# Kernel tuning notes

Hardware: AMD Instinct MI355X
Metric: run time of the kernel (lower is better)

Reference implementation:

```python
import jax, jax.numpy as jnp
import numpy as np

N = 256            # state_space_size
BF = (4, 4, 4)     # branching_factors
T = 128            # time steps
D_IN = 64          # input_size
D_T = 64           # time_embedding_size
BATCH = 16
NUM_NODES = N * 4 * 4 * 4  # 16384


def setup_inputs() -> dict:
    key = jax.random.key(0)
    ks = jax.random.split(key, 20)

    def lin_w(k, out_d, in_d):
        return jax.random.normal(k, (out_d, in_d), jnp.float32) / np.sqrt(in_d)

    inp = {
        "x": jax.random.normal(ks[0], (BATCH, T, N), jnp.float32),
        "t_embeddings_schedule": jax.random.normal(ks[1], (T, D_T), jnp.float32),
        "input_vector": jax.random.normal(ks[2], (BATCH, T, D_IN), jnp.float32),
        # Fanout node params
        "Wa": lin_w(ks[3], NUM_NODES, N),
        "ba": jnp.zeros((NUM_NODES,), jnp.float32),
        "Wt": lin_w(ks[4], NUM_NODES, D_T),
        "Wi": lin_w(ks[5], NUM_NODES, D_IN),
        # Node with bf[:3]=[4,4,4]: reduces last 4 -> [N,4,4]
        "w3": jax.random.normal(ks[6], (N, 4, 4, 4), jnp.float32) * np.sqrt(2.0 / (4 + N * 16)),
        "tW3": lin_w(ks[7], N * 16, D_T),
        "tb3": jnp.zeros((N * 16,), jnp.float32),
        # Node with bf[:2]=[4,4]
        "w2": jax.random.normal(ks[8], (N, 4, 4), jnp.float32) * np.sqrt(2.0 / (4 + N * 4)),
        "tW2": lin_w(ks[9], N * 4, D_T),
        "tb2": jnp.zeros((N * 4,), jnp.float32),
        # Node with bf[:1]=[4]
        "w1": jax.random.normal(ks[10], (N, 4), jnp.float32) * np.sqrt(2.0 / (4 + N)),
        "tW1": lin_w(ks[11], N, D_T),
        "tb1": jnp.zeros((N,), jnp.float32),
    }
    return inp


def _node(act, t_emb, w, tW, tb):
    # act: [..., T, N, *bf]; w: [N, *bf]; reduce last branching dim
    tproj = (t_emb @ tW.T + tb).reshape(t_emb.shape[0], *w.shape[:-1])  # [T, N, *bf[:-1]]
    pre = (w * act).sum(-1) + tproj  # broadcast over leading batch dims
    return jax.nn.softplus(pre)


def reference(x, t_embeddings_schedule, input_vector, Wa, ba, Wt, Wi,
              w3, tW3, tb3, w2, tW2, tb2, w1, tW1, tb1):
    t_emb = t_embeddings_schedule
    # Fanout: [B, T, N] -> [B, T, N, 4, 4, 4]
    pre = x @ Wa.T + ba + (t_emb @ Wt.T) + input_vector @ Wi.T  # [B, T, NUM_NODES]
    act = jax.nn.softplus(pre.reshape(*pre.shape[:-1], N, *BF))
    # Tree: deepest node first (insert-at-1 order in original)
    act = _node(act, t_emb, w3, tW3, tb3)  # [B, T, N, 4, 4]
    act = _node(act, t_emb, w2, tW2, tb2)  # [B, T, N, 4]
    act = _node(act, t_emb, w1, tW1, tb1)  # [B, T, N]
    return act
```

## Files before the change

kernel.cpp:

```cpp
#include <hip/hip_runtime.h>

typedef __attribute__((ext_vector_type(16))) float f32x16;
typedef __attribute__((ext_vector_type(8))) __bf16 bf16x8;
typedef __attribute__((ext_vector_type(8))) unsigned short u16x8;

__device__ __forceinline__ unsigned short f2bf(float f) {
    unsigned int u = __float_as_uint(f);
    u += 0x7fffu + ((u >> 16) & 1u);
    return (unsigned short)(u >> 16);
}

__device__ __forceinline__ float softplus_f(float x) {
    float e = __expf(-fabsf(x));
    return fmaf(__log2f(1.0f + e), 0.69314718056f, fmaxf(x, 0.0f));
}

typedef __attribute__((address_space(3))) void lds_void_t;
typedef __attribute__((address_space(1))) void glb_void_t;

__device__ __forceinline__ void load16_to_lds(const void* g, const void* l) {
    __builtin_amdgcn_global_load_lds((glb_void_t*)(unsigned long long)g,
                                     (lds_void_t*)(unsigned int)(unsigned long long)l,
                                     16, 0, 0);
}

#define REPACK_NB 2
#define REPACK_BLOCKS 1728
__global__ __launch_bounds__(256) void repack(
        const float* __restrict__ x, const float* __restrict__ iv,
        const float* __restrict__ temb,
        const float* __restrict__ Wa, const float* __restrict__ Wi,
        const float* __restrict__ Wt,
        unsigned short* __restrict__ Abf ) {
    const int stride = REPACK_BLOCKS * 256;
    const int tid0 = blockIdx.x * 256 + threadIdx.x;
    float4 f[REPACK_NB][2];
    #pragma unroll
    for (int c = 0; c < REPACK_NB; ++c) {
        const int idx = tid0 + c * stride;
        const bool isA = idx < 98304;
        const int widx = isA ? idx : idx - 98304;
        const int row = widx / 48;
        const int kk  = (widx % 48) * 8;
        const float* p0 = isA ? (x    + (size_t)row * 256) : (Wa + (size_t)row * 256);
        const float* p1 = isA ? (iv   + (size_t)row * 64)  : (Wi + (size_t)row * 64);
        const float* p2 = isA ? (temb + (size_t)(row & 127) * 64) : (Wt + (size_t)row * 64);
        const float* src = (kk < 256) ? (p0 + kk) : ((kk < 320) ? (p1 + kk - 256) : (p2 + kk - 320));
        f[c][0] = ((const float4*)src)[0];
        f[c][1] = ((const float4*)src)[1];
    }
    #pragma unroll
    for (int c = 0; c < REPACK_NB; ++c) {
        const int idx = tid0 + c * stride;
        const bool isA = idx < 98304;
        const int widx = isA ? idx : idx - 98304;
        const int row = widx / 48;
        const int ch  = widx % 48;
        const size_t dst = isA ? (size_t)(((row >> 5) * 48 + ch) * 32 + (row & 31))
                               : (size_t)idx;
        u16x8 o;
        o[0] = f2bf(f[c][0].x); o[1] = f2bf(f[c][0].y); o[2] = f2bf(f[c][0].z); o[3] = f2bf(f[c][0].w);
        o[4] = f2bf(f[c][1].x); o[5] = f2bf(f[c][1].y); o[6] = f2bf(f[c][1].z); o[7] = f2bf(f[c][1].w);
        *(u16x8*)(Abf + dst * 8) = o;
    }
}

__global__ __launch_bounds__(256) void tproj(
        const float* __restrict__ temb,
        const float* __restrict__ tW3, const float* __restrict__ tb3,
        const float* __restrict__ tW2, const float* __restrict__ tb2,
        const float* __restrict__ tW1, const float* __restrict__ tb1,
        float* __restrict__ tp3T, float* __restrict__ tp2T, float* __restrict__ tp1T) {
    __shared__ float se[32 * 64];
    const int tid = threadIdx.x;
    const int tbase = blockIdx.y * 32;
    for (int i = tid; i < 32 * 64; i += 256) se[i] = temb[tbase * 64 + i];
    __syncthreads();
    const int j = blockIdx.x * 64 + (tid >> 2);
    const float* W; const float* bias; float* outp; int jl;
    if      (j < 4096) { W = tW3; bias = tb3; outp = tp3T; jl = j; }
    else if (j < 5120) { W = tW2; bias = tb2; outp = tp2T; jl = j - 4096; }
    else               { W = tW1; bias = tb1; outp = tp1T; jl = j - 5120; }
    float4 wreg[16];
    const float4* wrow = (const float4*)(W + (size_t)jl * 64);
    #pragma unroll
    for (int k = 0; k < 16; ++k) wreg[k] = wrow[k];
    const float b = bias[jl];
    #pragma unroll
    for (int s = 0; s < 8; ++s) {
        const int tl = (tid & 3) + s * 4;
        const float4* e4 = (const float4*)&se[tl * 64];
        float a = b;
        #pragma unroll
        for (int k = 0; k < 16; ++k) {
            float4 e = e4[k];
            a += wreg[k].x * e.x + wreg[k].y * e.y + wreg[k].z * e.z + wreg[k].w * e.w;
        }
        outp[(size_t)jl * 128 + tbase + tl] = a;
    }
}

__global__ __launch_bounds__(256, 3)
void fused_gemm_tree(const unsigned short* __restrict__ Wbf,
                     const unsigned short* __restrict__ Abf,
                     const float* __restrict__ ba,
                     const float* __restrict__ tp3T, const float* __restrict__ tp2T,
                     const float* __restrict__ tp1T,
                     const float* __restrict__ w3, const float* __restrict__ w2,
                     const float* __restrict__ w1,
                     float* __restrict__ out) {
    __shared__ unsigned short sW[128 * 64];

    const int tid  = threadIdx.x;
    const int wave = tid >> 6;
    const int lane = tid & 63;
    const int wr = wave >> 1;
    const int wc = wave & 1;
    const int lane31 = lane & 31;
    const int h = lane >> 5;

    const int node0 = blockIdx.x * 128;
    const int m0    = blockIdx.y * 128;

    f32x16 acc[2][2];
    #pragma unroll
    for (int fm = 0; fm < 2; ++fm)
        #pragma unroll
        for (int s2 = 0; s2 < 4; ++s2) {
            const float4 b4 = *(const float4*)&ba[node0 + wr * 64 + fm * 32 + 8 * s2 + 4 * h];
            #pragma unroll
            for (int l = 0; l < 4; ++l) {
                acc[fm][0][s2 * 4 + l] = ((const float*)&b4)[l];
                acc[fm][1][s2 * 4 + l] = ((const float*)&b4)[l];
            }
        }

    const unsigned short* aBase = Wbf + (size_t)node0 * 384;
    const int wrow0 = wr * 64 + lane31;

    const int mtBase = blockIdx.y * 4 + wc * 2;
    const unsigned short* bC0 = Abf + (((size_t)(mtBase + 0) * 48 + h) * 32 + lane31) * 8;
    const unsigned short* bC1 = Abf + (((size_t)(mtBase + 1) * 48 + h) * 32 + lane31) * 8;

    for (int k0 = 0; k0 < 384; k0 += 64) {
        __syncthreads();
        #pragma unroll
        for (int rr = 0; rr < 4; ++rr) {
            const int p = rr * 256 + tid;
            const int row = p >> 3;
            const int kchunk = (p & 7) ^ (row & 7);
            load16_to_lds(aBase + (size_t)row * 384 + k0 + kchunk * 8,
                          &sW[(size_t)(rr * 256 + wave * 64) * 8]);
        }
        bf16x8 bfr[2][4];
        const int cbase = k0 >> 3;
        #pragma unroll
        for (int s = 0; s < 4; ++s) {
            bfr[0][s] = *(const bf16x8*)(bC0 + (size_t)(cbase + 2 * s) * 256);
            bfr[1][s] = *(const bf16x8*)(bC1 + (size_t)(cbase + 2 * s) * 256);
        }
        __syncthreads();

        #pragma unroll
        for (int s = 0; s < 4; ++s) {
            const int kc = s * 2 + h;
            const int slot = (kc ^ (lane31 & 7)) * 8;
            bf16x8 af[2];
            #pragma unroll
            for (int fm = 0; fm < 2; ++fm)
                af[fm] = *(const bf16x8*)&sW[(wrow0 + fm * 32) * 64 + slot];
            #pragma unroll
            for (int fm = 0; fm < 2; ++fm)
                #pragma unroll
                for (int cf = 0; cf < 2; ++cf)
                    acc[fm][cf] = __builtin_amdgcn_mfma_f32_32x32x16_bf16(af[fm], bfr[cf][s], acc[fm][cf], 0, 0, 0);
        }
    }

    const int n = blockIdx.x * 2 + wr;
    const int t0 = wc * 64 + lane31;

    float4 w3v[2][4];
    #pragma unroll
    for (int fm = 0; fm < 2; ++fm)
        #pragma unroll
        for (int s2 = 0; s2 < 4; ++s2)
            w3v[fm][s2] = *(const float4*)&w3[n * 64 + fm * 32 + 8 * s2 + 4 * h];

    float w2v[4][2], w1v[4];
    #pragma unroll
    for (int i = 0; i < 4; ++i) {
        #pragma unroll
        for (int s2b = 0; s2b < 2; ++s2b)
            w2v[i][s2b] = w2[n * 16 + i * 4 + 2 * s2b + h];
        w1v[i] = w1[n * 4 + i];
    }
    float tp3v[2][2][4];
    #pragma unroll
    for (int fm = 0; fm < 2; ++fm)
        #pragma unroll
        for (int cf = 0; cf < 2; ++cf) {
            const int t = t0 + cf * 32;
            #pragma unroll
            for (int s2 = 0; s2 < 4; ++s2) {
                const int i  = fm * 2 + (s2 >> 1);
                const int jj = 2 * (s2 & 1) + h;
                tp3v[fm][cf][s2] = tp3T[(size_t)((n * 4 + i) * 4 + jj) * 128 + t];
            }
        }
    const int th = t0 + h * 32;
    float tp2h[2][2];
    #pragma unroll
    for (int fm = 0; fm < 2; ++fm)
        #pragma unroll
        for (int b = 0; b < 2; ++b)
            tp2h[fm][b] = tp2T[(size_t)(n * 4 + fm * 2 + b) * 128 + th];
    const float tp1h = tp1T[(size_t)n * 128 + th];

    float s1h = 0.0f;
    #pragma unroll
    for (int fm = 0; fm < 2; ++fm) {
        #pragma unroll
        for (int b = 0; b < 2; ++b) {
            float cs[2];
            #pragma unroll
            for (int cf = 0; cf < 2; ++cf) {
                float c = 0.0f;
                #pragma unroll
                for (int s2b = 0; s2b < 2; ++s2b) {
                    const int s2 = 2 * b + s2b;
                    float p3 = 0.0f;
                    const float* wv = (const float*)&w3v[fm][s2];
                    #pragma unroll
                    for (int l = 0; l < 4; ++l) {
                        float a0 = softplus_f(acc[fm][cf][s2 * 4 + l]);
                        p3 = fmaf(a0, wv[l], p3);
                    }
                    float a3 = softplus_f(p3 + tp3v[fm][cf][s2]);
                    c = fmaf(a3, w2v[fm * 2 + b][s2b], c);
                }
                cs[cf] = c;
            }
            const float Q0 = cs[0] + __shfl_xor(cs[0], 32);
            const float Q1 = cs[1] + __shfl_xor(cs[1], 32);
            const float Qh = h ? Q1 : Q0;
            const float a2 = softplus_f(Qh + tp2h[fm][b]);
            s1h = fmaf(a2, w1v[fm * 2 + b], s1h);
        }
    }
    out[(size_t)(m0 + th) * 256 + n] = softplus_f(s1h + tp1h);
}

extern "C" void kernel_launch(void* const* d_in, const int* in_sizes, int n_in,
                              void* d_out, int out_size, void* d_ws, size_t ws_size,
                              hipStream_t stream) {
    const float* x    = (const float*)d_in[0];
    const float* temb = (const float*)d_in[1];
    const float* iv   = (const float*)d_in[2];
    const float* Wa   = (const float*)d_in[3];
    const float* ba   = (const float*)d_in[4];
    const float* Wt   = (const float*)d_in[5];
    const float* Wi   = (const float*)d_in[6];
    const float* w3   = (const float*)d_in[7];
    const float* tW3  = (const float*)d_in[8];
    const float* tb3  = (const float*)d_in[9];
    const float* w2   = (const float*)d_in[10];
    const float* tW2  = (const float*)d_in[11];
    const float* tb2  = (const float*)d_in[12];
    const float* w1   = (const float*)d_in[13];
    const float* tW1  = (const float*)d_in[14];
    const float* tb1  = (const float*)d_in[15];
    float* out = (float*)d_out;

    char* ws = (char*)d_ws;
    unsigned short* Abf = (unsigned short*)(ws);
    unsigned short* Wbf = (unsigned short*)(ws + 1572864);
    float* tp3T = (float*)(ws + 14155776);
    float* tp2T = (float*)(ws + 16252928);
    float* tp1T = (float*)(ws + 16777216);

    repack<<<dim3(REPACK_BLOCKS), dim3(256), 0, stream>>>(x, iv, temb, Wa, Wi, Wt, Abf);
    tproj<<<dim3(84, 4), dim3(256), 0, stream>>>(temb, tW3, tb3, tW2, tb2, tW1, tb1,
                                                 tp3T, tp2T, tp1T);
    fused_gemm_tree<<<dim3(128, 16), dim3(256), 0, stream>>>(Wbf, Abf, ba, tp3T, tp2T, tp1T,
                                                             w3, w2, w1, out);
}
```

Measured before the change: 149.3 us.

## Tile-pack weights in repack and feed MFMA from global, merge prep kernels

Merges the repack and tproj kernels into one prep launch. Prep now writes the weight matrix in the same 32-row tiled layout as the activations. With that layout the GEMM loads both operands straight from global memory into registers and drops the LDS staging and its barriers. The aim is to cut launch overhead and synchronisation, at the cost of losing LDS reuse of weight tiles across the waves in a block, which puts more load on L2.

After: 173.5 us. 16.2% more time.

```diff
diff --git a/kernel.cpp b/kernel.cpp
--- a/kernel.cpp
+++ b/kernel.cpp
@@ -15,25 +15,56 @@
     return fmaf(__log2f(1.0f + e), 0.69314718056f, fmaxf(x, 0.0f));
 }
 
-typedef __attribute__((address_space(3))) void lds_void_t;
-typedef __attribute__((address_space(1))) void glb_void_t;
-
-__device__ __forceinline__ void load16_to_lds(const void* g, const void* l) {
-    __builtin_amdgcn_global_load_lds((glb_void_t*)(unsigned long long)g,
-                                     (lds_void_t*)(unsigned int)(unsigned long long)l,
-                                     16, 0, 0);
-}
-
 #define REPACK_NB 2
 #define REPACK_BLOCKS 1728
-__global__ __launch_bounds__(256) void repack(
+#define TPROJ_BLOCKS 336
+#define PREP_BLOCKS (REPACK_BLOCKS + TPROJ_BLOCKS)
+__global__ __launch_bounds__(256) void prep(
         const float* __restrict__ x, const float* __restrict__ iv,
         const float* __restrict__ temb,
         const float* __restrict__ Wa, const float* __restrict__ Wi,
         const float* __restrict__ Wt,
-        unsigned short* __restrict__ Abf ) {
+        const float* __restrict__ tW3, const float* __restrict__ tb3,
+        const float* __restrict__ tW2, const float* __restrict__ tb2,
+        const float* __restrict__ tW1, const float* __restrict__ tb1,
+        unsigned short* __restrict__ Abf ,
+        float* __restrict__ tp3T, float* __restrict__ tp2T, float* __restrict__ tp1T) {
+    __shared__ float se[32 * 64];
+    const int tid = threadIdx.x;
+
+    if (blockIdx.x < TPROJ_BLOCKS) {
+        const int bx = blockIdx.x % 84;
+        const int by = blockIdx.x / 84;
+        const int tbase = by * 32;
+        for (int i = tid; i < 32 * 64; i += 256) se[i] = temb[tbase * 64 + i];
+        __syncthreads();
+        const int j = bx * 64 + (tid >> 2);
+        const float* W; const float* bias; float* outp; int jl;
+        if      (j < 4096) { W = tW3; bias = tb3; outp = tp3T; jl = j; }
+        else if (j < 5120) { W = tW2; bias = tb2; outp = tp2T; jl = j - 4096; }
+        else               { W = tW1; bias = tb1; outp = tp1T; jl = j - 5120; }
+        float4 wreg[16];
+        const float4* wrow = (const float4*)(W + (size_t)jl * 64);
+        #pragma unroll
+        for (int k = 0; k < 16; ++k) wreg[k] = wrow[k];
+        const float b = bias[jl];
+        #pragma unroll
+        for (int s = 0; s < 8; ++s) {
+            const int tl = (tid & 3) + s * 4;
+            const float4* e4 = (const float4*)&se[tl * 64];
+            float a = b;
+            #pragma unroll
+            for (int k = 0; k < 16; ++k) {
+                float4 e = e4[k];
+                a += wreg[k].x * e.x + wreg[k].y * e.y + wreg[k].z * e.z + wreg[k].w * e.w;
+            }
+            outp[(size_t)jl * 128 + tbase + tl] = a;
+        }
+        return;
+    }
+
     const int stride = REPACK_BLOCKS * 256;
-    const int tid0 = blockIdx.x * 256 + threadIdx.x;
+    const int tid0 = (blockIdx.x - TPROJ_BLOCKS) * 256 + tid;
     float4 f[REPACK_NB][2];
     #pragma unroll
     for (int c = 0; c < REPACK_NB; ++c) {
@@ -56,8 +87,8 @@
         const int widx = isA ? idx : idx - 98304;
         const int row = widx / 48;
         const int ch  = widx % 48;
-        const size_t dst = isA ? (size_t)(((row >> 5) * 48 + ch) * 32 + (row & 31))
-                               : (size_t)idx;
+        const size_t dst = (size_t)(isA ? 0 : 98304) +
+                           (size_t)(((row >> 5) * 48 + ch) * 32 + (row & 31));
         u16x8 o;
         o[0] = f2bf(f[c][0].x); o[1] = f2bf(f[c][0].y); o[2] = f2bf(f[c][0].z); o[3] = f2bf(f[c][0].w);
         o[4] = f2bf(f[c][1].x); o[5] = f2bf(f[c][1].y); o[6] = f2bf(f[c][1].z); o[7] = f2bf(f[c][1].w);
@@ -65,52 +96,15 @@
     }
 }
 
-__global__ __launch_bounds__(256) void tproj(
-        const float* __restrict__ temb,
-        const float* __restrict__ tW3, const float* __restrict__ tb3,
-        const float* __restrict__ tW2, const float* __restrict__ tb2,
-        const float* __restrict__ tW1, const float* __restrict__ tb1,
-        float* __restrict__ tp3T, float* __restrict__ tp2T, float* __restrict__ tp1T) {
-    __shared__ float se[32 * 64];
-    const int tid = threadIdx.x;
-    const int tbase = blockIdx.y * 32;
-    for (int i = tid; i < 32 * 64; i += 256) se[i] = temb[tbase * 64 + i];
-    __syncthreads();
-    const int j = blockIdx.x * 64 + (tid >> 2);
-    const float* W; const float* bias; float* outp; int jl;
-    if      (j < 4096) { W = tW3; bias = tb3; outp = tp3T; jl = j; }
-    else if (j < 5120) { W = tW2; bias = tb2; outp = tp2T; jl = j - 4096; }
-    else               { W = tW1; bias = tb1; outp = tp1T; jl = j - 5120; }
-    float4 wreg[16];
-    const float4* wrow = (const float4*)(W + (size_t)jl * 64);
-    #pragma unroll
-    for (int k = 0; k < 16; ++k) wreg[k] = wrow[k];
-    const float b = bias[jl];
-    #pragma unroll
-    for (int s = 0; s < 8; ++s) {
-        const int tl = (tid & 3) + s * 4;
-        const float4* e4 = (const float4*)&se[tl * 64];
-        float a = b;
-        #pragma unroll
-        for (int k = 0; k < 16; ++k) {
-            float4 e = e4[k];
-            a += wreg[k].x * e.x + wreg[k].y * e.y + wreg[k].z * e.z + wreg[k].w * e.w;
-        }
-        outp[(size_t)jl * 128 + tbase + tl] = a;
-    }
-}
-
 __global__ __launch_bounds__(256, 3)
-void fused_gemm_tree(const unsigned short* __restrict__ Wbf,
-                     const unsigned short* __restrict__ Abf,
+void fused_gemm_tree(const unsigned short* __restrict__ Wf,
+                     const unsigned short* __restrict__ Af,
                      const float* __restrict__ ba,
                      const float* __restrict__ tp3T, const float* __restrict__ tp2T,
                      const float* __restrict__ tp1T,
                      const float* __restrict__ w3, const float* __restrict__ w2,
                      const float* __restrict__ w1,
                      float* __restrict__ out) {
-    __shared__ unsigned short sW[128 * 64];
-
     const int tid  = threadIdx.x;
     const int wave = tid >> 6;
     const int lane = tid & 63;
@@ -135,46 +129,24 @@
             }
         }
 
-    const unsigned short* aBase = Wbf + (size_t)node0 * 384;
-    const int wrow0 = wr * 64 + lane31;
-
+    const int ntBase = blockIdx.x * 4 + wr * 2;
     const int mtBase = blockIdx.y * 4 + wc * 2;
-    const unsigned short* bC0 = Abf + (((size_t)(mtBase + 0) * 48 + h) * 32 + lane31) * 8;
-    const unsigned short* bC1 = Abf + (((size_t)(mtBase + 1) * 48 + h) * 32 + lane31) * 8;
-
-    for (int k0 = 0; k0 < 384; k0 += 64) {
-        __syncthreads();
-        #pragma unroll
-        for (int rr = 0; rr < 4; ++rr) {
-            const int p = rr * 256 + tid;
-            const int row = p >> 3;
-            const int kchunk = (p & 7) ^ (row & 7);
-            load16_to_lds(aBase + (size_t)row * 384 + k0 + kchunk * 8,
-                          &sW[(size_t)(rr * 256 + wave * 64) * 8]);
-        }
-        bf16x8 bfr[2][4];
-        const int cbase = k0 >> 3;
-        #pragma unroll
-        for (int s = 0; s < 4; ++s) {
-            bfr[0][s] = *(const bf16x8*)(bC0 + (size_t)(cbase + 2 * s) * 256);
-            bfr[1][s] = *(const bf16x8*)(bC1 + (size_t)(cbase + 2 * s) * 256);
-        }
-        __syncthreads();
-
-        #pragma unroll
-        for (int s = 0; s < 4; ++s) {
-            const int kc = s * 2 + h;
-            const int slot = (kc ^ (lane31 & 7)) * 8;
-            bf16x8 af[2];
-            #pragma unroll
-            for (int fm = 0; fm < 2; ++fm)
-                af[fm] = *(const bf16x8*)&sW[(wrow0 + fm * 32) * 64 + slot];
-            #pragma unroll
-            for (int fm = 0; fm < 2; ++fm)
-                #pragma unroll
-                for (int cf = 0; cf < 2; ++cf)
-                    acc[fm][cf] = __builtin_amdgcn_mfma_f32_32x32x16_bf16(af[fm], bfr[cf][s], acc[fm][cf], 0, 0, 0);
-        }
+    const unsigned short* aC0 = Wf + (((size_t)(ntBase + 0) * 48 + h) * 32 + lane31) * 8;
+    const unsigned short* aC1 = Wf + (((size_t)(ntBase + 1) * 48 + h) * 32 + lane31) * 8;
+    const unsigned short* bC0 = Af + (((size_t)(mtBase + 0) * 48 + h) * 32 + lane31) * 8;
+    const unsigned short* bC1 = Af + (((size_t)(mtBase + 1) * 48 + h) * 32 + lane31) * 8;
+
+    #pragma unroll
+    for (int c = 0; c < 48; c += 2) {
+        const size_t off = (size_t)c * 256;
+        bf16x8 a0 = *(const bf16x8*)(aC0 + off);
+        bf16x8 a1 = *(const bf16x8*)(aC1 + off);
+        bf16x8 b0 = *(const bf16x8*)(bC0 + off);
+        bf16x8 b1 = *(const bf16x8*)(bC1 + off);
+        acc[0][0] = __builtin_amdgcn_mfma_f32_32x32x16_bf16(a0, b0, acc[0][0], 0, 0, 0);
+        acc[0][1] = __builtin_amdgcn_mfma_f32_32x32x16_bf16(a0, b1, acc[0][1], 0, 0, 0);
+        acc[1][0] = __builtin_amdgcn_mfma_f32_32x32x16_bf16(a1, b0, acc[1][0], 0, 0, 0);
+        acc[1][1] = __builtin_amdgcn_mfma_f32_32x32x16_bf16(a1, b1, acc[1][1], 0, 0, 0);
     }
 
     const int n = blockIdx.x * 2 + wr;
@@ -279,9 +251,9 @@
     float* tp2T = (float*)(ws + 16252928);
     float* tp1T = (float*)(ws + 16777216);
 
-    repack<<<dim3(REPACK_BLOCKS), dim3(256), 0, stream>>>(x, iv, temb, Wa, Wi, Wt, Abf);
-    tproj<<<dim3(84, 4), dim3(256), 0, stream>>>(temb, tW3, tb3, tW2, tb2, tW1, tb1,
-                                                 tp3T, tp2T, tp1T);
+    prep<<<dim3(PREP_BLOCKS), dim3(256), 0, stream>>>(x, iv, temb, Wa, Wi, Wt,
+                                                      tW3, tb3, tW2, tb2, tW1, tb1,
+                                                      Abf, tp3T, tp2T, tp1T);
     fused_gemm_tree<<<dim3(128, 16), dim3(256), 0, stream>>>(Wbf, Abf, ba, tp3T, tp2T, tp1T,
                                                              w3, w2, w1, out);
 }
```

## Double-buffer LDS in GEMM loop and fuse repack with tproj kernel

Applied to the files above, without the earlier changes.

The GEMM main loop now uses two LDS buffers, issuing the async global-to-LDS load for the next K tile before computing on the current one, and drops one barrier per iteration. The repack and time-projection kernels are merged into a single launch with block-index dispatch, saving a launch and letting both run concurrently. LDS usage per block doubles, which could affect occupancy.

After: 143.8 us. -3.7%, faster.

```diff
diff --git a/kernel.cpp b/kernel.cpp
--- a/kernel.cpp
+++ b/kernel.cpp
@@ -26,14 +26,54 @@
 
 #define REPACK_NB 2
 #define REPACK_BLOCKS 1728
-__global__ __launch_bounds__(256) void repack(
+#define TPROJ_BLOCKS 336
+#define PREP_BLOCKS (REPACK_BLOCKS + TPROJ_BLOCKS)
+__global__ __launch_bounds__(256) void prep(
         const float* __restrict__ x, const float* __restrict__ iv,
         const float* __restrict__ temb,
         const float* __restrict__ Wa, const float* __restrict__ Wi,
         const float* __restrict__ Wt,
-        unsigned short* __restrict__ Abf ) {
+        const float* __restrict__ tW3, const float* __restrict__ tb3,
+        const float* __restrict__ tW2, const float* __restrict__ tb2,
+        const float* __restrict__ tW1, const float* __restrict__ tb1,
+        unsigned short* __restrict__ Abf ,
+        float* __restrict__ tp3T, float* __restrict__ tp2T, float* __restrict__ tp1T) {
+    __shared__ float se[32 * 64];
+    const int tid = threadIdx.x;
+
+    if (blockIdx.x < TPROJ_BLOCKS) {
+        const int bx = blockIdx.x % 84;
+        const int by = blockIdx.x / 84;
+        const int tbase = by * 32;
+        for (int i = tid; i < 32 * 64; i += 256) se[i] = temb[tbase * 64 + i];
+        __syncthreads();
+        const int j = bx * 64 + (tid >> 2);
+        const float* W; const float* bias; float* outp; int jl;
+        if      (j < 4096) { W = tW3; bias = tb3; outp = tp3T; jl = j; }
+        else if (j < 5120) { W = tW2; bias = tb2; outp = tp2T; jl = j - 4096; }
+        else               { W = tW1; bias = tb1; outp = tp1T; jl = j - 5120; }
+        float4 wreg[16];
+        const float4* wrow = (const float4*)(W + (size_t)jl * 64);
+        #pragma unroll
+        for (int k = 0; k < 16; ++k) wreg[k] = wrow[k];
+        const float b = bias[jl];
+        #pragma unroll
+        for (int s = 0; s < 8; ++s) {
+            const int tl = (tid & 3) + s * 4;
+            const float4* e4 = (const float4*)&se[tl * 64];
+            float a = b;
+            #pragma unroll
+            for (int k = 0; k < 16; ++k) {
+                float4 e = e4[k];
+                a += wreg[k].x * e.x + wreg[k].y * e.y + wreg[k].z * e.z + wreg[k].w * e.w;
+            }
+            outp[(size_t)jl * 128 + tbase + tl] = a;
+        }
+        return;
+    }
+
     const int stride = REPACK_BLOCKS * 256;
-    const int tid0 = blockIdx.x * 256 + threadIdx.x;
+    const int tid0 = (blockIdx.x - TPROJ_BLOCKS) * 256 + tid;
     float4 f[REPACK_NB][2];
     #pragma unroll
     for (int c = 0; c < REPACK_NB; ++c) {
@@ -65,41 +105,6 @@
     }
 }
 
-__global__ __launch_bounds__(256) void tproj(
-        const float* __restrict__ temb,
-        const float* __restrict__ tW3, const float* __restrict__ tb3,
-        const float* __restrict__ tW2, const float* __restrict__ tb2,
-        const float* __restrict__ tW1, const float* __restrict__ tb1,
-        float* __restrict__ tp3T, float* __restrict__ tp2T, float* __restrict__ tp1T) {
-    __shared__ float se[32 * 64];
-    const int tid = threadIdx.x;
-    const int tbase = blockIdx.y * 32;
-    for (int i = tid; i < 32 * 64; i += 256) se[i] = temb[tbase * 64 + i];
-    __syncthreads();
-    const int j = blockIdx.x * 64 + (tid >> 2);
-    const float* W; const float* bias; float* outp; int jl;
-    if      (j < 4096) { W = tW3; bias = tb3; outp = tp3T; jl = j; }
-    else if (j < 5120) { W = tW2; bias = tb2; outp = tp2T; jl = j - 4096; }
-    else               { W = tW1; bias = tb1; outp = tp1T; jl = j - 5120; }
-    float4 wreg[16];
-    const float4* wrow = (const float4*)(W + (size_t)jl * 64);
-    #pragma unroll
-    for (int k = 0; k < 16; ++k) wreg[k] = wrow[k];
-    const float b = bias[jl];
-    #pragma unroll
-    for (int s = 0; s < 8; ++s) {
-        const int tl = (tid & 3) + s * 4;
-        const float4* e4 = (const float4*)&se[tl * 64];
-        float a = b;
-        #pragma unroll
-        for (int k = 0; k < 16; ++k) {
-            float4 e = e4[k];
-            a += wreg[k].x * e.x + wreg[k].y * e.y + wreg[k].z * e.z + wreg[k].w * e.w;
-        }
-        outp[(size_t)jl * 128 + tbase + tl] = a;
-    }
-}
-
 __global__ __launch_bounds__(256, 3)
 void fused_gemm_tree(const unsigned short* __restrict__ Wbf,
                      const unsigned short* __restrict__ Abf,
@@ -109,7 +114,7 @@
                      const float* __restrict__ w3, const float* __restrict__ w2,
                      const float* __restrict__ w1,
                      float* __restrict__ out) {
-    __shared__ unsigned short sW[128 * 64];
+    __shared__ unsigned short sW[2][128 * 64];
 
     const int tid  = threadIdx.x;
     const int wave = tid >> 6;
@@ -142,16 +147,25 @@
     const unsigned short* bC0 = Abf + (((size_t)(mtBase + 0) * 48 + h) * 32 + lane31) * 8;
     const unsigned short* bC1 = Abf + (((size_t)(mtBase + 1) * 48 + h) * 32 + lane31) * 8;
 
-    for (int k0 = 0; k0 < 384; k0 += 64) {
-        __syncthreads();
-        #pragma unroll
-        for (int rr = 0; rr < 4; ++rr) {
-            const int p = rr * 256 + tid;
-            const int row = p >> 3;
-            const int kchunk = (p & 7) ^ (row & 7);
-            load16_to_lds(aBase + (size_t)row * 384 + k0 + kchunk * 8,
-                          &sW[(size_t)(rr * 256 + wave * 64) * 8]);
-        }
+    int srow[4], skch[4];
+    #pragma unroll
+    for (int rr = 0; rr < 4; ++rr) {
+        const int p = rr * 256 + tid;
+        srow[rr] = p >> 3;
+        skch[rr] = (p & 7) ^ (srow[rr] & 7);
+    }
+    #define STAGE_A(K0, BB)                                                        \
+        _Pragma("unroll")                                                          \
+        for (int rr = 0; rr < 4; ++rr)                                             \
+            load16_to_lds(aBase + (size_t)srow[rr] * 384 + (K0) + skch[rr] * 8,    \
+                          &sW[BB][(size_t)(rr * 256 + wave * 64) * 8]);
+
+    STAGE_A(0, 0);
+    __syncthreads();
+
+    #pragma unroll
+    for (int it = 0; it < 6; ++it) {
+        const int k0 = it * 64;
         bf16x8 bfr[2][4];
         const int cbase = k0 >> 3;
         #pragma unroll
@@ -159,22 +173,21 @@
             bfr[0][s] = *(const bf16x8*)(bC0 + (size_t)(cbase + 2 * s) * 256);
             bfr[1][s] = *(const bf16x8*)(bC1 + (size_t)(cbase + 2 * s) * 256);
         }
-        __syncthreads();
-
+        if (it < 5) { STAGE_A(k0 + 64, (it + 1) & 1); }
         #pragma unroll
         for (int s = 0; s < 4; ++s) {
             const int kc = s * 2 + h;
-            const int slot = (kc ^ (lane31 & 7)) * 8;
+            const int slot = (kc ^ (lane & 7)) * 8;
             bf16x8 af[2];
             #pragma unroll
             for (int fm = 0; fm < 2; ++fm)
-                af[fm] = *(const bf16x8*)&sW[(wrow0 + fm * 32) * 64 + slot];
-            #pragma unroll
-            for (int fm = 0; fm < 2; ++fm)
-                #pragma unroll
-                for (int cf = 0; cf < 2; ++cf)
-                    acc[fm][cf] = __builtin_amdgcn_mfma_f32_32x32x16_bf16(af[fm], bfr[cf][s], acc[fm][cf], 0, 0, 0);
-        }
+                af[fm] = *(const bf16x8*)&sW[it & 1][(wrow0 + fm * 32) * 64 + slot];
+            acc[0][0] = __builtin_amdgcn_mfma_f32_32x32x16_bf16(af[0], bfr[0][s], acc[0][0], 0, 0, 0);
+            acc[0][1] = __builtin_amdgcn_mfma_f32_32x32x16_bf16(af[0], bfr[1][s], acc[0][1], 0, 0, 0);
+            acc[1][0] = __builtin_amdgcn_mfma_f32_32x32x16_bf16(af[1], bfr[0][s], acc[1][0], 0, 0, 0);
+            acc[1][1] = __builtin_amdgcn_mfma_f32_32x32x16_bf16(af[1], bfr[1][s], acc[1][1], 0, 0, 0);
+        }
+        if (it < 5) __syncthreads();
     }
 
     const int n = blockIdx.x * 2 + wr;
@@ -279,9 +292,9 @@
     float* tp2T = (float*)(ws + 16252928);
     float* tp1T = (float*)(ws + 16777216);
 
-    repack<<<dim3(REPACK_BLOCKS), dim3(256), 0, stream>>>(x, iv, temb, Wa, Wi, Wt, Abf);
-    tproj<<<dim3(84, 4), dim3(256), 0, stream>>>(temb, tW3, tb3, tW2, tb2, tW1, tb1,
-                                                 tp3T, tp2T, tp1T);
+    prep<<<dim3(PREP_BLOCKS), dim3(256), 0, stream>>>(x, iv, temb, Wa, Wi, Wt,
+                                                      tW3, tb3, tW2, tb2, tW1, tb1,
+                                                      Abf, tp3T, tp2T, tp1T);
     fused_gemm_tree<<<dim3(128, 16), dim3(256), 0, stream>>>(Wbf, Abf, ba, tp3T, tp2T, tp1T,
                                                              w3, w2, w1, out);
 }
```
